# Kernel tuning notes

Hardware: AMD Instinct MI355X
Metric: run time of the kernel (lower is better)

## Reference

```python
import jax, jax.numpy as jnp
import numpy as np

B = 256        # graphs (documents) per batch
NPG = 200      # nodes per graph
EPG = 1600     # edges per graph (~2*ngram+2 per token)
D = 200        # hidden_size_node (glove.6B.200d)
V = 50000      # vocab size
ENUM = 2000000 # global edge-id vocabulary
C = 20         # class_num
N = B * NPG
E = B * EPG


def setup_inputs() -> dict:
    key = jax.random.key(0)
    ks = jax.random.split(key, 8)
    node_ids = jax.random.randint(ks[0], (N,), 0, V, dtype=jnp.int32)
    # graph-local endpoints + per-graph node offset (mimics dgl.batch)
    src_local = jax.random.randint(ks[1], (E,), 0, NPG, dtype=jnp.int32)
    dst_local = jax.random.randint(ks[2], (E,), 0, NPG, dtype=jnp.int32)
    off = jnp.repeat(jnp.arange(B, dtype=jnp.int32) * NPG, EPG)
    edge_src = src_local + off
    edge_dst = dst_local + off
    edge_ids = jax.random.randint(ks[3], (E,), 0, ENUM, dtype=jnp.int32)
    node_seg = jnp.repeat(jnp.arange(B, dtype=jnp.int32), NPG)
    node_emb = jax.random.normal(ks[4], (V, D), dtype=jnp.float32) * 0.1
    # trainable_edges=True -> edge weight table initialized to ones
    edge_w = jnp.ones((ENUM, 1), dtype=jnp.float32)
    W = jax.random.normal(ks[5], (D, C), dtype=jnp.float32) * 0.05
    b = jnp.zeros((C,), dtype=jnp.float32)
    return {"node_emb": node_emb, "edge_w": edge_w, "W": W, "b": b,
            "node_ids": node_ids, "edge_src": edge_src, "edge_dst": edge_dst,
            "edge_ids": edge_ids, "node_seg": node_seg}


def reference(node_emb, edge_w, W, b, node_ids, edge_src, edge_dst, edge_ids, node_seg):
    h = node_emb[node_ids]                       # [N, D] node hidden states
    msg = h[edge_src] * edge_w[edge_ids]         # [E, D] src feat * edge weight
    # scatter-max reduce onto destination nodes (dgl max reduce)
    h_max = jax.ops.segment_max(msg, edge_dst, num_segments=N)
    h_max = jnp.where(jnp.isfinite(h_max), h_max, jnp.float32(0.0))  # empty segs -> 0 like DGL
    pooled = jax.ops.segment_sum(h_max, node_seg, num_segments=B)   # dgl.sum_nodes -> [B, D]
    # dropout is identity in eval / p=0.0
    return jax.nn.relu(pooled) @ W + b           # [B, C]
```

## Files before the change

kernel.cpp:

```cpp
#include <hip/hip_runtime.h>

#define NPG 200
#define EPG 1600
#define DIM 200
#define NCLS 20
#define NGRAPH 256
#define THREADS 1024
#define NWAVES 16
#define NPB 100
#define Q4 50
#define NEG_INF (-__builtin_inff())

__global__ __launch_bounds__(THREADS, 8) void gnn_gather(
    const float* __restrict__ node_emb,
    const float* __restrict__ edge_w,
    const int*   __restrict__ node_ids,
    const int*   __restrict__ edge_src,
    const int*   __restrict__ edge_dst,
    const int*   __restrict__ edge_ids,
    float*       __restrict__ partial)
{
    __shared__ int            nidb[NPG];
    __shared__ unsigned short srcl[EPG];
    __shared__ unsigned short dstl[EPG];
    __shared__ float          wv[EPG];
    __shared__ uint2          ce[EPG];
    __shared__ int            csum[128];
    __shared__ int            cursor[NPB];
    __shared__ short          wstart[NWAVES + 1];
    __shared__ float          part[NWAVES][DIM];

    const int bid = blockIdx.x;
    const int g   = bid & (NGRAPH - 1);
    const int h   = bid >> 8;
    const int n0g = h * NPB;
    const int tid = threadIdx.x;
    const int gbase_n = g * NPG;
    const int gbase_e = g * EPG;

    if (tid < NPG) nidb[tid] = node_ids[gbase_n + tid] * (DIM * 4);
    if (tid < 128) csum[tid] = 0;
    __syncthreads();

    for (int e = tid; e < EPG; e += THREADS) {
        int s  = edge_src[gbase_e + e] - gbase_n;
        int dl = edge_dst[gbase_e + e] - gbase_n;
        srcl[e] = (unsigned short)s;
        dstl[e] = (unsigned short)dl;
        int n = dl - n0g;
        if ((unsigned)n < NPB) {
            wv[e] = edge_w[edge_ids[gbase_e + e]];
            atomicAdd(&csum[n], 1);
        }
    }
    __syncthreads();

    if (tid < 64) {
        int2 c = *reinterpret_cast<int2*>(&csum[tid * 2]);
        int s1 = c.x + c.y;
        int carry = s1;
        #pragma unroll
        for (int off = 1; off < 64; off <<= 1) {
            int t = __shfl_up(carry, off);
            if (tid >= off) carry += t;
        }
        int base = carry - s1;
        int2 o; o.x = base + c.x; o.y = base + s1;
        *reinterpret_cast<int2*>(&csum[tid * 2]) = o;
    }
    __syncthreads();

    const int total = csum[NPB - 1];
    if (tid < NPB) cursor[tid] = (tid == 0) ? 0 : csum[tid - 1];
    if (tid <= NWAVES) {
        int target = (tid * total) >> 4;
        int lo = 0, hi = NPB;
        while (lo < hi) {
            int mid = (lo + hi) >> 1;
            int excl = mid ? csum[mid - 1] : 0;
            if (excl >= target) hi = mid; else lo = mid + 1;
        }
        wstart[tid] = (short)lo;
    }
    __syncthreads();

    for (int e = tid; e < EPG; e += THREADS) {
        int n = (int)dstl[e] - n0g;
        if ((unsigned)n < NPB) {
            int excl = n ? csum[n - 1] : 0;
            int pos  = atomicAdd(&cursor[n], 1);
            unsigned pack = (unsigned)nidb[srcl[e]] | (pos == excl ? 1u : 0u);
            ce[pos] = make_uint2(pack, __float_as_uint(wv[e]));
        }
    }
    __syncthreads();

    const int w    = tid >> 6;
    const int lane = tid & 63;
    if (lane < Q4) {
        const int a0 = wstart[w];
        const int a1 = wstart[w + 1];
        const int kb = a0 ? csum[a0 - 1] : 0;
        const int ke = a1 ? csum[a1 - 1] : 0;
        const char* lb = (const char*)node_emb + lane * 16;

        float4 p = make_float4(0.f, 0.f, 0.f, 0.f);
        float4 m = make_float4(0.f, 0.f, 0.f, 0.f);

        #pragma unroll 8
        for (int k = kb; k < ke; ++k) {
            const uint2 q2  = ce[k];
            const bool  ns  = (q2.x & 1u);
            const float wgt = __uint_as_float(q2.y);
            const float4 v  = *reinterpret_cast<const float4*>(lb + (q2.x & ~1u));
            p.x += ns ? m.x : 0.0f;  p.y += ns ? m.y : 0.0f;
            p.z += ns ? m.z : 0.0f;  p.w += ns ? m.w : 0.0f;
            m.x = fmaxf(ns ? NEG_INF : m.x, v.x * wgt);
            m.y = fmaxf(ns ? NEG_INF : m.y, v.y * wgt);
            m.z = fmaxf(ns ? NEG_INF : m.z, v.z * wgt);
            m.w = fmaxf(ns ? NEG_INF : m.w, v.w * wgt);
        }
        p.x += m.x; p.y += m.y; p.z += m.z; p.w += m.w;
        *reinterpret_cast<float4*>(&part[w][lane * 4]) = p;
    }
    __syncthreads();

    if (tid < DIM) {
        float t = 0.f;
        #pragma unroll
        for (int i = 0; i < NWAVES; ++i) t += part[i][tid];
        partial[(h * NGRAPH + g) * DIM + tid] = t;
    }
}

__global__ __launch_bounds__(256) void gnn_head(
    const float* __restrict__ partial,
    const float* __restrict__ Wm,
    const float* __restrict__ bv,
    float*       __restrict__ out)
{
    __shared__ float pooled[DIM];
    __shared__ float Ws[DIM * NCLS];
    const int g   = blockIdx.x;
    const int tid = threadIdx.x;

    for (int i = tid; i < DIM * NCLS; i += 256) Ws[i] = Wm[i];
    if (tid < DIM) {
        float s = partial[g * DIM + tid] + partial[(NGRAPH + g) * DIM + tid];
        pooled[tid] = fmaxf(s, 0.0f);
    }
    __syncthreads();

    if (tid < NCLS) {
        float acc = bv[tid];
        #pragma unroll 4
        for (int k = 0; k < DIM; ++k)
            acc += pooled[k] * Ws[k * NCLS + tid];
        out[g * NCLS + tid] = acc;
    }
}

extern "C" void kernel_launch(void* const* d_in, const int* in_sizes, int n_in,
                              void* d_out, int out_size, void* d_ws, size_t ws_size,
                              hipStream_t stream) {
    const float* node_emb = (const float*)d_in[0];
    const float* edge_w   = (const float*)d_in[1];
    const float* Wm       = (const float*)d_in[2];
    const float* bv       = (const float*)d_in[3];
    const int*   node_ids = (const int*)d_in[4];
    const int*   edge_src = (const int*)d_in[5];
    const int*   edge_dst = (const int*)d_in[6];
    const int*   edge_ids = (const int*)d_in[7];

    float* partial = (float*)d_ws;

    gnn_gather<<<2 * NGRAPH, THREADS, 0, stream>>>(node_emb, edge_w,
                                                   node_ids, edge_src, edge_dst, edge_ids,
                                                   partial);
    gnn_head<<<NGRAPH, 256, 0, stream>>>(partial, Wm, bv, (float*)d_out);
}
```

Before: 126.5 us.

## Precompute per-node bf16 embedding rows in a compact graph-local buffer

Adds a pre-pass kernel that gathers each node's embedding row via node_ids, rounds it to bf16 and writes it into a dense per-graph buffer in workspace. The gather kernel then indexes by graph-local source node, reading 8-byte bf16 pairs instead of 16-byte fp32 vectors, which halves the bytes per edge and gives locality within a graph's 200 rows. The head kernel also reads W directly instead of staging it in shared memory. The cost is an extra launch plus a write and re-read of a 41 MB intermediate, and bf16 rounding of the embeddings can add precision error.

```diff
diff --git a/kernel.cpp b/kernel.cpp
--- a/kernel.cpp
+++ b/kernel.cpp
@@ -5,22 +5,40 @@
 #define DIM 200
 #define NCLS 20
 #define NGRAPH 256
+#define ROWU 100
+#define ROWB 400
 #define THREADS 1024
 #define NWAVES 16
 #define NPB 100
 #define Q4 50
 #define NEG_INF (-__builtin_inff())
 
+__global__ __launch_bounds__(256) void emb_cache(
+    const float* __restrict__ node_emb,
+    const int*   __restrict__ node_ids,
+    unsigned*    __restrict__ emb16,
+    int total)
+{
+    int i = blockIdx.x * 256 + threadIdx.x;
+    const int stride = gridDim.x * 256;
+    for (; i < total; i += stride) {
+        const int n = i / ROWU;
+        const int c = i - n * ROWU;
+        const float2 v = *reinterpret_cast<const float2*>(
+            node_emb + (size_t)node_ids[n] * DIM + c * 2);
+        emb16[i] = ((__float_as_uint(v.y) + 0x8000u) & 0xffff0000u) |
+                   ((__float_as_uint(v.x) + 0x8000u) >> 16);
+    }
+}
+
 __global__ __launch_bounds__(THREADS, 8) void gnn_gather(
-    const float* __restrict__ node_emb,
-    const float* __restrict__ edge_w,
-    const int*   __restrict__ node_ids,
-    const int*   __restrict__ edge_src,
-    const int*   __restrict__ edge_dst,
-    const int*   __restrict__ edge_ids,
-    float*       __restrict__ partial)
+    const unsigned* __restrict__ emb16,
+    const float*    __restrict__ edge_w,
+    const int*      __restrict__ edge_src,
+    const int*      __restrict__ edge_dst,
+    const int*      __restrict__ edge_ids,
+    float*          __restrict__ partial)
 {
-    __shared__ int            nidb[NPG];
     __shared__ unsigned short srcl[EPG];
     __shared__ unsigned short dstl[EPG];
     __shared__ float          wv[EPG];
@@ -38,7 +56,6 @@
     const int gbase_n = g * NPG;
     const int gbase_e = g * EPG;
 
-    if (tid < NPG) nidb[tid] = node_ids[gbase_n + tid] * (DIM * 4);
     if (tid < 128) csum[tid] = 0;
     __syncthreads();
 
@@ -89,7 +106,7 @@
         if ((unsigned)n < NPB) {
             int excl = n ? csum[n - 1] : 0;
             int pos  = atomicAdd(&cursor[n], 1);
-            unsigned pack = (unsigned)nidb[srcl[e]] | (pos == excl ? 1u : 0u);
+            unsigned pack = (unsigned)srcl[e] * ROWB | (pos == excl ? 1u : 0u);
             ce[pos] = make_uint2(pack, __float_as_uint(wv[e]));
         }
     }
@@ -102,7 +119,7 @@
         const int a1 = wstart[w + 1];
         const int kb = a0 ? csum[a0 - 1] : 0;
         const int ke = a1 ? csum[a1 - 1] : 0;
-        const char* lb = (const char*)node_emb + lane * 16;
+        const char* lb = (const char*)emb16 + (size_t)g * (NPG * ROWB) + lane * 8;
 
         float4 p = make_float4(0.f, 0.f, 0.f, 0.f);
         float4 m = make_float4(0.f, 0.f, 0.f, 0.f);
@@ -112,13 +129,17 @@
             const uint2 q2  = ce[k];
             const bool  ns  = (q2.x & 1u);
             const float wgt = __uint_as_float(q2.y);
-            const float4 v  = *reinterpret_cast<const float4*>(lb + (q2.x & ~1u));
+            const uint2 rv  = *reinterpret_cast<const uint2*>(lb + (q2.x & ~1u));
+            const float c0 = __uint_as_float(rv.x << 16)         * wgt;
+            const float c1 = __uint_as_float(rv.x & 0xffff0000u) * wgt;
+            const float c2 = __uint_as_float(rv.y << 16)         * wgt;
+            const float c3 = __uint_as_float(rv.y & 0xffff0000u) * wgt;
             p.x += ns ? m.x : 0.0f;  p.y += ns ? m.y : 0.0f;
             p.z += ns ? m.z : 0.0f;  p.w += ns ? m.w : 0.0f;
-            m.x = fmaxf(ns ? NEG_INF : m.x, v.x * wgt);
-            m.y = fmaxf(ns ? NEG_INF : m.y, v.y * wgt);
-            m.z = fmaxf(ns ? NEG_INF : m.z, v.z * wgt);
-            m.w = fmaxf(ns ? NEG_INF : m.w, v.w * wgt);
+            m.x = fmaxf(ns ? NEG_INF : m.x, c0);
+            m.y = fmaxf(ns ? NEG_INF : m.y, c1);
+            m.z = fmaxf(ns ? NEG_INF : m.z, c2);
+            m.w = fmaxf(ns ? NEG_INF : m.w, c3);
         }
         p.x += m.x; p.y += m.y; p.z += m.z; p.w += m.w;
         *reinterpret_cast<float4*>(&part[w][lane * 4]) = p;
@@ -129,7 +150,7 @@
         float t = 0.f;
         #pragma unroll
         for (int i = 0; i < NWAVES; ++i) t += part[i][tid];
-        partial[(h * NGRAPH + g) * DIM + tid] = t;
+        partial[bid * DIM + tid] = t;
     }
 }
 
@@ -140,11 +161,9 @@
     float*       __restrict__ out)
 {
     __shared__ float pooled[DIM];
-    __shared__ float Ws[DIM * NCLS];
     const int g   = blockIdx.x;
     const int tid = threadIdx.x;
 
-    for (int i = tid; i < DIM * NCLS; i += 256) Ws[i] = Wm[i];
     if (tid < DIM) {
         float s = partial[g * DIM + tid] + partial[(NGRAPH + g) * DIM + tid];
         pooled[tid] = fmaxf(s, 0.0f);
@@ -155,7 +174,7 @@
         float acc = bv[tid];
         #pragma unroll 4
         for (int k = 0; k < DIM; ++k)
-            acc += pooled[k] * Ws[k * NCLS + tid];
+            acc += pooled[k] * Wm[k * NCLS + tid];
         out[g * NCLS + tid] = acc;
     }
 }
@@ -172,10 +191,15 @@
     const int*   edge_dst = (const int*)d_in[6];
     const int*   edge_ids = (const int*)d_in[7];
 
-    float* partial = (float*)d_ws;
-
-    gnn_gather<<<2 * NGRAPH, THREADS, 0, stream>>>(node_emb, edge_w,
-                                                   node_ids, edge_src, edge_dst, edge_ids,
+    const int N = in_sizes[4];
+    const int total_u32 = N * ROWU;
+
+    unsigned* emb16   = (unsigned*)d_ws;
+    float*    partial = (float*)d_ws + (size_t)total_u32;
+
+    emb_cache<<<2048, 256, 0, stream>>>(node_emb, node_ids, emb16, total_u32);
+    gnn_gather<<<2 * NGRAPH, THREADS, 0, stream>>>(emb16, edge_w,
+                                                   edge_src, edge_dst, edge_ids,
                                                    partial);
     gnn_head<<<NGRAPH, 256, 0, stream>>>(partial, Wm, bv, (float*)d_out);
 }
```

Measured after the change: 143.0 us. 1.13x slower.
